# Kernel optimization log

Measured on AMD Instinct MI355X. Metric: run time of the kernel, lower is better.

Reference implementation:

```python
import jax, jax.numpy as jnp
import numpy as np

LOG2PI = float(np.log(2.0 * np.pi))
EPS_SHIFT = -0.5   # self.eps
TAU = 0.5          # self.tau
ETA = 1.0          # self.eta
MAG_A = 5500.0     # magnitude remap constants from forward()
MAG_B = 1100.0


def setup_inputs() -> dict:
    key = jax.random.key(0)
    k1, k2, k3, k4, k5 = jax.random.split(key, 5)
    B, K, C = 4096, 128, 64
    z = jax.random.normal(k1, (B, K, 2), dtype=jnp.float32)
    # per-keypoint mixture weights summing to 1 (GMM weights_)
    weights = jax.nn.softmax(jax.random.normal(k2, (K, C), dtype=jnp.float32), axis=-1)
    means = jax.random.normal(k3, (K, C, 2), dtype=jnp.float32)
    # SPD covariances: A A^T + 0.2 I
    A = jax.random.normal(k4, (K, C, 2, 2), dtype=jnp.float32) * 0.3
    covs = jnp.einsum('kcij,kclj->kcil', A, A) + 0.2 * jnp.eye(2, dtype=jnp.float32)
    # latent_stats unnormalization factor per latent coordinate (2/(max-min))
    scale = jax.random.uniform(k5, (K, 2), dtype=jnp.float32, minval=0.5, maxval=2.0)
    return {"z": z, "weights": weights, "means": means, "covs": covs, "scale": scale}


def _gmm_pdf_and_grad(z, weights, means, covs):
    # z: [B,K,2]  weights: [K,C]  means: [K,C,2]  covs: [K,C,2,2]
    a = covs[..., 0, 0]; b = covs[..., 0, 1]
    c = covs[..., 1, 0]; d = covs[..., 1, 1]
    det = a * d - b * c                                  # [K,C]
    inv00 = d / det; inv01 = -b / det
    inv10 = -c / det; inv11 = a / det
    diff = z[:, :, None, :] - means[None]                # [B,K,C,2]
    d0 = diff[..., 0]; d1 = diff[..., 1]
    s0 = inv00 * d0 + inv01 * d1                         # Sigma^{-1} diff, [B,K,C]
    s1 = inv10 * d0 + inv11 * d1
    maha = d0 * s0 + d1 * s1                             # [B,K,C]
    logp = -0.5 * (maha + jnp.log(det) + 2.0 * LOG2PI)   # MVN log_prob (D=2)
    comp = weights[None] * jnp.exp(logp)                 # weighted component densities
    pdf = comp.sum(-1)                                   # [B,K]
    # analytic grad of pdf wrt z: sum_c comp_c * (-Sigma_c^{-1} (z-mu_c))
    g0 = -(comp * s0).sum(-1)
    g1 = -(comp * s1).sum(-1)
    grad = jnp.stack([g0, g1], axis=-1)                  # [B,K,2]
    return pdf, grad


def reference(z, weights, means, covs, scale):
    B, K, _ = z.shape
    pdf, grad = _gmm_pdf_and_grad(z, weights, means, covs)
    # densities duplicated per coordinate: [pdf_i, pdf_i] per keypoint -> [B, 2K]
    densities = jnp.repeat(pdf, 2, axis=-1)
    density_norm = jax.nn.sigmoid((densities + EPS_SHIFT) / TAU)
    # unnormalize_gradient: elementwise rescale into raw latent space
    grad_raw = grad * scale[None]                        # [B,K,2]
    nrm = jnp.linalg.norm(grad_raw, axis=-1, keepdims=True)  # [B,K,1]
    mag = jnp.exp((-nrm + MAG_A) / MAG_B)
    negexp_grad = (grad_raw / nrm) * mag                 # [B,K,2]
    return density_norm, ETA * negexp_grad.reshape(B, 2 * K)
```

## Files before the change

kernel.cpp:

```cpp
#include <hip/hip_runtime.h>

#define K_KP   128
#define C_COMP 64
#define TK     8
#define TBS    32
#define NB     4
#define LDS_STRIDE 388

typedef float v2f __attribute__((ext_vector_type(2)));

#if __has_builtin(__builtin_amdgcn_exp2f)
#define EXP2F(x) __builtin_amdgcn_exp2f(x)
#else
#define EXP2F(x) exp2f(x)
#endif
#if __has_builtin(__builtin_amdgcn_logf)
#define LOG2F_(x) __builtin_amdgcn_logf(x)
#else
#define LOG2F_(x) __log2f(x)
#endif
#if __has_builtin(__builtin_amdgcn_rcpf)
#define RCPF(x) __builtin_amdgcn_rcpf(x)
#else
#define RCPF(x) (1.0f/(x))
#endif
#if __has_builtin(__builtin_amdgcn_rsqf)
#define RSQF(x) __builtin_amdgcn_rsqf(x)
#else
#define RSQF(x) rsqrtf(x)
#endif

#define EVAL(m0, m1, i00, i01, i11, lc, ZX, ZY, PDF, G0, G1)            \
    {                                                                   \
        v2f d0 = ZX - (m0);                                             \
        v2f d1 = ZY - (m1);                                             \
        v2f s0 = (i00) * d0 + (i01) * d1;   \
        v2f s1 = (i01) * d0 + (i11) * d1;                               \
        v2f arg = (lc) - d0 * s0 - d1 * s1;           \
        v2f e;                                                          \
        e.x = EXP2F(arg.x);                                             \
        e.y = EXP2F(arg.y);                                             \
        PDF += e;                                                       \
        G0 += e * s0;                                                   \
        G1 += e * s1;                                                   \
    }

__global__ __launch_bounds__(256, 4) void recovery_kernel(
    const float* __restrict__ z,
    const float* __restrict__ weights,
    const float* __restrict__ means,
    const float* __restrict__ covs,
    const float* __restrict__ scale,
    float* __restrict__ out, int B)
{
    __shared__ float lds[TK * LDS_STRIDE];

    const int t  = threadIdx.x;
    const int kb = blockIdx.x & 15;
    const int bb = blockIdx.x >> 4;
    const int k0 = kb * TK;
    const int b0 = bb * (TBS * NB);

    const float K2       = 0.72134752044f;
    const float LOG2_2PI = 2.6514961295f;
    for (int i = t; i < TK * C_COMP; i += 256) {
        int kl = i >> 6;
        int c  = i & 63;
        int g  = (k0 + kl) * C_COMP + c;
        float w  = weights[g];
        float m0 = means[2*g], m1 = means[2*g + 1];
        float a  = covs[4*g],     bq = covs[4*g + 1];
        float cq = covs[4*g + 2], d  = covs[4*g + 3];
        float det  = a*d - bq*cq;
        float rdet = RCPF(det);
        float i00 = d  * rdet * K2;
        float i01 = -bq * rdet * K2;
        float i11 = a  * rdet * K2;
        float lc = LOG2F_(w) - LOG2_2PI - 0.5f * LOG2F_(det);
        float* row = &lds[kl * LDS_STRIDE + (c >> 1) * 12];
        ((float4*)(row + (c & 1) * 4))[0] = make_float4(m0, m1, i00, i01);
        ((float2*)(row + 8 + (c & 1) * 2))[0] = make_float2(i11, lc);
    }
    __syncthreads();

    const int kl = t & 7;
    const int bl = t >> 3;
    const int kg = k0 + kl;

    const float2* z2 = (const float2*)z;
    float zx[NB], zy[NB];
#pragma unroll
    for (int j = 0; j < NB; ++j) {
        int b = b0 + bl + j * TBS;
        float2 v = z2[(size_t)b * K_KP + kg];
        zx[j] = v.x; zy[j] = v.y;
    }

    v2f ZXa = {zx[0], zx[1]}, ZXb = {zx[2], zx[3]};
    v2f ZYa = {zy[0], zy[1]}, ZYb = {zy[2], zy[3]};
    v2f pdfa = {0.f, 0.f}, pdfb = {0.f, 0.f};
    v2f g0a  = {0.f, 0.f}, g0b  = {0.f, 0.f};
    v2f g1a  = {0.f, 0.f}, g1b  = {0.f, 0.f};

    const float* kp = &lds[kl * LDS_STRIDE];
#pragma unroll 4
    for (int p = 0; p < C_COMP / 2; ++p) {
        float4 A0 = *(const float4*)(kp + p * 12);
        float4 A1 = *(const float4*)(kp + p * 12 + 4);
        float4 Bp = *(const float4*)(kp + p * 12 + 8);
        EVAL(A0.x, A0.y, A0.z, A0.w, Bp.x, Bp.y, ZXa, ZYa, pdfa, g0a, g1a);
        EVAL(A0.x, A0.y, A0.z, A0.w, Bp.x, Bp.y, ZXb, ZYb, pdfb, g0b, g1b);
        EVAL(A1.x, A1.y, A1.z, A1.w, Bp.z, Bp.w, ZXa, ZYa, pdfa, g0a, g1a);
        EVAL(A1.x, A1.y, A1.z, A1.w, Bp.z, Bp.w, ZXb, ZYb, pdfb, g0b, g1b);
    }

    float pdf[NB] = {pdfa.x, pdfa.y, pdfb.x, pdfb.y};
    float gs0[NB] = {g0a.x, g0a.y, g0b.x, g0b.y};
    float gs1[NB] = {g1a.x, g1a.y, g1b.x, g1b.y};

    float2 sc = ((const float2*)scale)[kg];
    const float NEG_INV_K2 = -1.3862943611f;
    float f0 = sc.x * NEG_INV_K2;
    float f1 = sc.y * NEG_INV_K2;
    const int KK2 = 2 * K_KP;
    float* out0 = out;
    float* out1 = out + (size_t)B * KK2;
#pragma unroll
    for (int j = 0; j < NB; ++j) {
        int b = b0 + bl + j * TBS;
        float x  = 2.0f * pdf[j] - 1.0f;
        float ex = EXP2F(-1.44269504f * x);
        float dn = RCPF(1.0f + ex);
        float g0 = gs0[j] * f0;
        float g1 = gs1[j] * f1;
        float n2 = fmaf(g0, g0, g1 * g1);
        float rn = RSQF(n2);
        float nrm = n2 * rn;
        float mag = EXP2F(fmaf(nrm, -0.0013115409f, 7.2134752044f));
        float m = rn * mag;
        ((float2*)(out0 + (size_t)b * KK2 + 2 * kg))[0] = make_float2(dn, dn);
        ((float2*)(out1 + (size_t)b * KK2 + 2 * kg))[0] = make_float2(g0 * m, g1 * m);
    }
}

extern "C" void kernel_launch(void* const* d_in, const int* in_sizes, int n_in,
                              void* d_out, int out_size, void* d_ws, size_t ws_size,
                              hipStream_t stream) {
    const float* z       = (const float*)d_in[0];
    const float* weights = (const float*)d_in[1];
    const float* means   = (const float*)d_in[2];
    const float* covs    = (const float*)d_in[3];
    const float* scale   = (const float*)d_in[4];
    float* out = (float*)d_out;

    int B = in_sizes[0] / (2 * K_KP);
    int grid = (K_KP / TK) * (B / (TBS * NB));
    recovery_kernel<<<grid, 256, 0, stream>>>(z, weights, means, covs, scale, out, B);
}
```

Measured before the change: 73.26 us.

## Halve per-thread batch work and hoist z loads before parameter staging

```diff
diff --git a/kernel.cpp b/kernel.cpp
--- a/kernel.cpp
+++ b/kernel.cpp
@@ -4,7 +4,7 @@
 #define C_COMP 64
 #define TK     8
 #define TBS    32
-#define NB     4
+#define NB     2
 #define LDS_STRIDE 388
 
 typedef float v2f __attribute__((ext_vector_type(2)));
@@ -61,12 +61,20 @@
     const int k0 = kb * TK;
     const int b0 = bb * (TBS * NB);
 
+    const int kl = t & 7;
+    const int bl = t >> 3;
+    const int kg = k0 + kl;
+
+    const float2* z2 = (const float2*)z;
+    float2 zv0 = z2[(size_t)(b0 + bl) * K_KP + kg];
+    float2 zv1 = z2[(size_t)(b0 + bl + TBS) * K_KP + kg];
+
     const float K2       = 0.72134752044f;
     const float LOG2_2PI = 2.6514961295f;
     for (int i = t; i < TK * C_COMP; i += 256) {
-        int kl = i >> 6;
+        int kr = i >> 6;
         int c  = i & 63;
-        int g  = (k0 + kl) * C_COMP + c;
+        int g  = (k0 + kr) * C_COMP + c;
         float w  = weights[g];
         float m0 = means[2*g], m1 = means[2*g + 1];
         float a  = covs[4*g],     bq = covs[4*g + 1];
@@ -77,46 +85,31 @@
         float i01 = -bq * rdet * K2;
         float i11 = a  * rdet * K2;
         float lc = LOG2F_(w) - LOG2_2PI - 0.5f * LOG2F_(det);
-        float* row = &lds[kl * LDS_STRIDE + (c >> 1) * 12];
+        float* row = &lds[kr * LDS_STRIDE + (c >> 1) * 12];
         ((float4*)(row + (c & 1) * 4))[0] = make_float4(m0, m1, i00, i01);
         ((float2*)(row + 8 + (c & 1) * 2))[0] = make_float2(i11, lc);
     }
     __syncthreads();
 
-    const int kl = t & 7;
-    const int bl = t >> 3;
-    const int kg = k0 + kl;
-
-    const float2* z2 = (const float2*)z;
-    float zx[NB], zy[NB];
-#pragma unroll
-    for (int j = 0; j < NB; ++j) {
-        int b = b0 + bl + j * TBS;
-        float2 v = z2[(size_t)b * K_KP + kg];
-        zx[j] = v.x; zy[j] = v.y;
-    }
-
-    v2f ZXa = {zx[0], zx[1]}, ZXb = {zx[2], zx[3]};
-    v2f ZYa = {zy[0], zy[1]}, ZYb = {zy[2], zy[3]};
-    v2f pdfa = {0.f, 0.f}, pdfb = {0.f, 0.f};
-    v2f g0a  = {0.f, 0.f}, g0b  = {0.f, 0.f};
-    v2f g1a  = {0.f, 0.f}, g1b  = {0.f, 0.f};
+    v2f ZX = {zv0.x, zv1.x};
+    v2f ZY = {zv0.y, zv1.y};
+    v2f pdfv = {0.f, 0.f};
+    v2f g0v  = {0.f, 0.f};
+    v2f g1v  = {0.f, 0.f};
 
     const float* kp = &lds[kl * LDS_STRIDE];
-#pragma unroll 4
+#pragma unroll 8
     for (int p = 0; p < C_COMP / 2; ++p) {
         float4 A0 = *(const float4*)(kp + p * 12);
         float4 A1 = *(const float4*)(kp + p * 12 + 4);
         float4 Bp = *(const float4*)(kp + p * 12 + 8);
-        EVAL(A0.x, A0.y, A0.z, A0.w, Bp.x, Bp.y, ZXa, ZYa, pdfa, g0a, g1a);
-        EVAL(A0.x, A0.y, A0.z, A0.w, Bp.x, Bp.y, ZXb, ZYb, pdfb, g0b, g1b);
-        EVAL(A1.x, A1.y, A1.z, A1.w, Bp.z, Bp.w, ZXa, ZYa, pdfa, g0a, g1a);
-        EVAL(A1.x, A1.y, A1.z, A1.w, Bp.z, Bp.w, ZXb, ZYb, pdfb, g0b, g1b);
+        EVAL(A0.x, A0.y, A0.z, A0.w, Bp.x, Bp.y, ZX, ZY, pdfv, g0v, g1v);
+        EVAL(A1.x, A1.y, A1.z, A1.w, Bp.z, Bp.w, ZX, ZY, pdfv, g0v, g1v);
     }
 
-    float pdf[NB] = {pdfa.x, pdfa.y, pdfb.x, pdfb.y};
-    float gs0[NB] = {g0a.x, g0a.y, g0b.x, g0b.y};
-    float gs1[NB] = {g1a.x, g1a.y, g1b.x, g1b.y};
+    float pdf[NB] = {pdfv.x, pdfv.y};
+    float gs0[NB] = {g0v.x, g0v.y};
+    float gs1[NB] = {g1v.x, g1v.y};
 
     float2 sc = ((const float2*)scale)[kg];
     const float NEG_INV_K2 = -1.3862943611f;
```

Result: no change. 74.57 us (+1.8%).
